# Optimization experiments

Measured on AMD Instinct MI355X. Metric: run time of the kernel, lower is better.

The kernel has to match this reference:

```python
import jax, jax.numpy as jnp
import numpy as np

B, D, E, K, NC, NH = 8192, 1280, 4, 2, 20, 4
CD = D // NC      # chunk_dim = 64
HD = CD // NH     # head_dim = 16
FF = CD * 4       # ffn hidden = 256
EPS = 1e-8


def setup_inputs() -> dict:
    key = jax.random.key(0)
    ks = jax.random.split(key, 12)
    f = lambda k, sh, s=0.02: jax.random.normal(k, sh, jnp.float32) * s
    return {
        "x": jax.random.normal(ks[0], (B, D), jnp.float32),
        "gate_w1": f(ks[1], (E * 4, D)), "gate_b1": jnp.zeros((E * 4,), jnp.float32),
        "gate_w2": f(ks[2], (E, E * 4)), "gate_b2": jnp.zeros((E,), jnp.float32),
        "pos_embed": f(ks[3], (E, NC, CD)),
        "norm1_g": jnp.ones((E, CD), jnp.float32),
        "in_proj_w": f(ks[4], (E, 3 * CD, CD)), "in_proj_b": jnp.zeros((E, 3 * CD), jnp.float32),
        "out_proj_w": f(ks[5], (E, CD, CD)), "out_proj_b": jnp.zeros((E, CD), jnp.float32),
        "ls1_g": jnp.full((E, CD), 1e-4, jnp.float32),
        "norm2_g": jnp.ones((E, CD), jnp.float32),
        "ffn_w1": f(ks[6], (E, FF, CD)), "ffn_b1": jnp.zeros((E, FF), jnp.float32),
        "ffn_w2": f(ks[7], (E, CD, FF)), "ffn_b2": jnp.zeros((E, CD), jnp.float32),
        "ls2_g": jnp.full((E, CD), 1e-4, jnp.float32),
        "proj_w": f(ks[8], (E, D, D)), "proj_b": jnp.zeros((E, D), jnp.float32),
    }


def _rms(v, g):
    # torch RMSNorm in source: x / (||x||_2 * dim^-0.5 + eps) * g
    n = jnp.linalg.norm(v, axis=-1, keepdims=True) * (CD ** -0.5)
    return v / (n + EPS) * g


def _expert(x, pos, n1g, ipw, ipb, opw, opb, l1, n2g, fw1, fb1, fw2, fb2, l2, pw, pb):
    b = x.shape[0]
    xs = x.reshape(b, NC, CD) + pos            # [b, NC, CD]
    xn = _rms(xs, n1g)
    qkv = xn @ ipw.T + ipb                      # [b, NC, 3*CD]
    q, k, v = jnp.split(qkv, 3, axis=-1)
    q = q.reshape(b, NC, NH, HD).transpose(0, 2, 1, 3)
    k = k.reshape(b, NC, NH, HD).transpose(0, 2, 1, 3)
    v = v.reshape(b, NC, NH, HD).transpose(0, 2, 1, 3)
    att = jax.nn.softmax(jnp.einsum('bhqd,bhkd->bhqk', q, k) * (HD ** -0.5), axis=-1)
    o = jnp.einsum('bhqk,bhkd->bhqd', att, v).transpose(0, 2, 1, 3).reshape(b, NC, CD)
    o = o @ opw.T + opb
    xs = xs + l1 * o                            # residual + LayerScale
    h = jax.nn.relu(_rms(xs, n2g) @ fw1.T + fb1) @ fw2.T + fb2
    xs = xs + l2 * h
    return xs.reshape(b, D) @ pw.T + pb         # final proj [b, D]


def reference(x, gate_w1, gate_b1, gate_w2, gate_b2, pos_embed, norm1_g,
              in_proj_w, in_proj_b, out_proj_w, out_proj_b, ls1_g, norm2_g,
              ffn_w1, ffn_b1, ffn_w2, ffn_b2, ls2_g, proj_w, proj_b):
    logits = jnp.tanh(x @ gate_w1.T + gate_b1) @ gate_w2.T + gate_b2   # [B, E]
    scores = jax.nn.softmax(logits, axis=-1)
    tk_s, tk_i = jax.lax.top_k(scores, K)
    tk_s = tk_s / (tk_s.sum(-1, keepdims=True) + 1e-6)
    onehot = jax.nn.one_hot(tk_i, E, dtype=x.dtype)                    # [B, K, E]
    w = (onehot * tk_s[..., None]).sum(1)                              # [B, E] combine weights
    eout = jax.vmap(_expert, in_axes=(None,) + (0,) * 15)(
        x, pos_embed, norm1_g, in_proj_w, in_proj_b, out_proj_w, out_proj_b,
        ls1_g, norm2_g, ffn_w1, ffn_b1, ffn_w2, ffn_b2, ls2_g, proj_w, proj_b)  # [E, B, D]
    output = jnp.einsum('ebd,be->bd', eout, w)
    aux_loss = jnp.float32(0.0)  # eval mode
    load = onehot.sum((0, 1))    # [E]
    return output, aux_loss, load
```

## Files before the change

### kernel.cpp

```cpp
#include <hip/hip_runtime.h>
#include <hip/hip_bf16.h>
#include <math.h>

#define B_SZ 8192
#define D_SZ 1280
#define NE   4
#define NC   20
#define CD   64
#define NH   4
#define HD   16
#define FF   256

typedef __attribute__((ext_vector_type(8))) short bf16x8;
typedef __attribute__((ext_vector_type(4))) float f32x4;

__device__ inline unsigned int pk2(float lo, float hi) {
    union { __hip_bfloat16 h; unsigned short s; } a, b;
    a.h = __float2bfloat16(lo); b.h = __float2bfloat16(hi);
    return (unsigned int)a.s | ((unsigned int)b.s << 16);
}
__device__ inline __hip_bfloat16 us2bf(unsigned short u) {
    union { unsigned short s; __hip_bfloat16 h; } c; c.s = u; return c.h;
}

#define WS_TOPI   256
#define WS_TOPW   (WS_TOPI + 2*B_SZ*4)
#define WS_IDX    (WS_TOPW + 2*B_SZ*4)
#define WS_WGT    (WS_IDX  + 2*B_SZ*4)
#define WS_ER0    (WS_WGT  + 2*B_SZ*4)
#define WS_ER1    (WS_ER0  + B_SZ*4)
#define WS_PRK    (WS_ER1  + B_SZ*4)
#define WS_BBE    (WS_PRK  + B_SZ*4)
#define WS_BBP    (WS_BBE  + 32*4*4)
#define WS_PRA    (WS_BBP  + 32*16*4)
#define WS_PRB    (WS_PRA  + (B_SZ+128)*4)
#define WS_PW1    (WS_PRB  + (B_SZ+128)*4)
#define WS_PW2    (WS_PW1  + (B_SZ+128)*4)
#define WS_PRW    (WS_PW2  + (B_SZ+128)*4)
#define WS_XSF    532480
#define XSF_ROWS  (2*B_SZ + 128)
#define WS_PWB    (WS_XSF + (size_t)XSF_ROWS * D_SZ * 2)
#define WS_IPWB   (WS_PWB  + (size_t)NE * D_SZ * D_SZ * 2)
#define WS_OPWB   (WS_IPWB + (size_t)NE * 192 * 64 * 2)
#define WS_FW1B   (WS_OPWB + (size_t)NE * 64 * 64 * 2)
#define WS_FW2B   (WS_FW1B + (size_t)NE * 256 * 64 * 2)

__global__ __launch_bounds__(256) void convert_pw(const float* __restrict__ pw,
                                                  __hip_bfloat16* __restrict__ pwb)
{
    size_t i = ((size_t)blockIdx.x * 256 + threadIdx.x) * 8;
    float4 a = *(const float4*)(pw + i);
    float4 b = *(const float4*)(pw + i + 4);
    __hip_bfloat16 h[8];
    h[0] = __float2bfloat16(a.x); h[1] = __float2bfloat16(a.y);
    h[2] = __float2bfloat16(a.z); h[3] = __float2bfloat16(a.w);
    h[4] = __float2bfloat16(b.x); h[5] = __float2bfloat16(b.y);
    h[6] = __float2bfloat16(b.z); h[7] = __float2bfloat16(b.w);
    *(uint4*)(pwb + i) = *(uint4*)h;
}

#define N_IPW (NE*192*64)
#define N_OPW (NE*64*64)
#define N_FW1 (NE*256*64)
#define N_FW2 (NE*64*256)
__global__ __launch_bounds__(256) void convert_small(
    const float* __restrict__ ipw, const float* __restrict__ opw,
    const float* __restrict__ fw1, const float* __restrict__ fw2,
    __hip_bfloat16* __restrict__ ipwb, __hip_bfloat16* __restrict__ opwb,
    __hip_bfloat16* __restrict__ fw1b, __hip_bfloat16* __restrict__ fw2b)
{
    size_t i = ((size_t)blockIdx.x * 256 + threadIdx.x) * 8;
    const float* src; __hip_bfloat16* dst; size_t off;
    if (i < N_IPW)                       { src = ipw; dst = ipwb; off = i; }
    else if (i < N_IPW + N_OPW)          { src = opw; dst = opwb; off = i - N_IPW; }
    else if (i < N_IPW + N_OPW + N_FW1)  { src = fw1; dst = fw1b; off = i - N_IPW - N_OPW; }
    else                                 { src = fw2; dst = fw2b; off = i - N_IPW - N_OPW - N_FW1; }
    float4 a = *(const float4*)(src + off);
    float4 b = *(const float4*)(src + off + 4);
    __hip_bfloat16 h[8];
    h[0] = __float2bfloat16(a.x); h[1] = __float2bfloat16(a.y);
    h[2] = __float2bfloat16(a.z); h[3] = __float2bfloat16(a.w);
    h[4] = __float2bfloat16(b.x); h[5] = __float2bfloat16(b.y);
    h[6] = __float2bfloat16(b.z); h[7] = __float2bfloat16(b.w);
    *(uint4*)(dst + off) = *(uint4*)h;
}

__global__ __launch_bounds__(64) void gate_kernel(
    const float* __restrict__ x, const float* __restrict__ gw1, const float* __restrict__ gb1,
    const float* __restrict__ gw2, const float* __restrict__ gb2,
    int* __restrict__ topi, float* __restrict__ topw)
{
    const int b = blockIdx.x;
    const int lane = threadIdx.x;
    float acc[16];
#pragma unroll
    for (int j = 0; j < 16; ++j) acc[j] = 0.f;
    const float* xr = x + (size_t)b * D_SZ;
    for (int t = 0; t < NC; ++t) {
        float xv = xr[t * 64 + lane];
#pragma unroll
        for (int j = 0; j < 16; ++j) acc[j] += xv * gw1[j * D_SZ + t * 64 + lane];
    }
#pragma unroll
    for (int j = 0; j < 16; ++j) {
        acc[j] += __shfl_xor(acc[j], 32, 64);
        acc[j] += __shfl_xor(acc[j], 16, 64);
        acc[j] += __shfl_xor(acc[j], 8, 64);
        acc[j] += __shfl_xor(acc[j], 4, 64);
        acc[j] += __shfl_xor(acc[j], 2, 64);
        acc[j] += __shfl_xor(acc[j], 1, 64);
    }
    if (lane == 0) {
        float h[16];
#pragma unroll
        for (int j = 0; j < 16; ++j) h[j] = tanhf(acc[j] + gb1[j]);
        float l[4];
#pragma unroll
        for (int e = 0; e < 4; ++e) {
            float sv = gb2[e];
#pragma unroll
            for (int j = 0; j < 16; ++j) sv += h[j] * gw2[e * 16 + j];
            l[e] = sv;
        }
        float m = fmaxf(fmaxf(l[0], l[1]), fmaxf(l[2], l[3]));
        float p[4];
        float sum = 0.f;
#pragma unroll
        for (int e = 0; e < 4; ++e) { p[e] = expf(l[e] - m); sum += p[e]; }
#pragma unroll
        for (int e = 0; e < 4; ++e) p[e] /= sum;
        int i1 = 0;
#pragma unroll
        for (int e = 1; e < 4; ++e) if (p[e] > p[i1]) i1 = e;
        int i2 = (i1 == 0) ? 1 : 0;
#pragma unroll
        for (int e = 0; e < 4; ++e) if (e != i1 && p[e] > p[i2]) i2 = e;
        float s1 = p[i1], s2 = p[i2];
        float denom = s1 + s2 + 1e-6f;
        topi[b * 2 + 0] = i1;
        topi[b * 2 + 1] = i2;
        topw[b * 2 + 0] = s1 / denom;
        topw[b * 2 + 1] = s2 / denom;
    }
}

__global__ __launch_bounds__(256) void count_kernel(
    const int* __restrict__ topi,
    int* __restrict__ cnt, int* __restrict__ pcnt,
    int* __restrict__ er0, int* __restrict__ er1, int* __restrict__ prk,
    int* __restrict__ bbe, int* __restrict__ bbp)
{
    __shared__ int he[4], hp[16];
    const int t = threadIdx.x;
    const int blk = blockIdx.x;
    const int b = blk * 256 + t;
    if (t < 4) he[t] = 0;
    if (t < 16) hp[t] = 0;
    __syncthreads();
    int e0 = topi[b * 2], e1 = topi[b * 2 + 1];
    er0[b] = atomicAdd(&he[e0], 1);
    er1[b] = atomicAdd(&he[e1], 1);
    prk[b] = atomicAdd(&hp[e0 * 4 + e1], 1);
    __syncthreads();
    if (t < 4)  bbe[blk * 4 + t]  = atomicAdd(&cnt[t], he[t]);
    if (t < 16) bbp[blk * 16 + t] = atomicAdd(&pcnt[t], hp[t]);
}

__global__ void offsets_kernel(const int* __restrict__ cnt, const int* __restrict__ pcnt,
                               int* __restrict__ offA, int* __restrict__ poff,
                               float* __restrict__ load_out)
{
    if (threadIdx.x == 0 && blockIdx.x == 0) {
        int a = 0;
#pragma unroll
        for (int e = 0; e < 4; ++e) { offA[e] = a; a += cnt[e]; }
        offA[4] = a;
        int q = 0;
#pragma unroll
        for (int p = 0; p < 16; ++p) { poff[p] = q; q += pcnt[p]; }
        poff[16] = q;
#pragma unroll
        for (int e = 0; e < 4; ++e) load_out[e] = (float)cnt[e];
    }
}

__global__ __launch_bounds__(256) void fill_kernel(
    const int* __restrict__ topi, const float* __restrict__ topw,
    const int* __restrict__ offA, const int* __restrict__ poff,
    const int* __restrict__ er0, const int* __restrict__ er1, const int* __restrict__ prk,
    const int* __restrict__ bbe, const int* __restrict__ bbp,
    int* __restrict__ idx_list, float* __restrict__ wgt_list,
    int* __restrict__ prA, int* __restrict__ prB,
    float* __restrict__ pw1, float* __restrict__ pw2, int* __restrict__ prow)
{
    const int b = blockIdx.x * 256 + threadIdx.x;
    const int blk = blockIdx.x;
    int e0 = topi[b * 2], e1 = topi[b * 2 + 1];
    float w0 = topw[b * 2], w1 = topw[b * 2 + 1];
    int slot0 = offA[e0] + bbe[blk * 4 + e0] + er0[b];
    int slot1 = offA[e1] + bbe[blk * 4 + e1] + er1[b];
    idx_list[slot0] = b; wgt_list[slot0] = w0;
    idx_list[slot1] = b; wgt_list[slot1] = w1;
    int p = e0 * 4 + e1;
    int pos = poff[p] + bbp[blk * 16 + p] + prk[b];
    prA[pos] = slot0; prB[pos] = slot1;
    pw1[pos] = w0; pw2[pos] = w1; prow[pos] = b;
}

__global__ __launch_bounds__(256, 5) void expert_inner(
    const float* __restrict__ x, const float* __restrict__ pos,
    const float* __restrict__ n1g,
    const __hip_bfloat16* __restrict__ ipwb, const float* __restrict__ ipb,
    const __hip_bfloat16* __restrict__ opwb, const float* __restrict__ opb,
    const float* __restrict__ ls1, const float* __restrict__ n2g,
    const __hip_bfloat16* __restrict__ fw1b, const float* __restrict__ fb1,
    const __hip_bfloat16* __restrict__ fw2b, const float* __restrict__ fb2,
    const float* __restrict__ ls2,
    const int* __restrict__ offA, const int* __restrict__ idx_list,
    const float* __restrict__ wgt_list,
    __hip_bfloat16* __restrict__ xsf)
{
    __shared__ __hip_bfloat16 s_big[4][32][72];

    const int t = threadIdx.x;
    const int w = t >> 6;
    const int lane = t & 63;
    const int l15 = lane & 15, lg = lane >> 4;
    const int s = blockIdx.x * 4 + w;
    const int e = (s >= offA[1]) + (s >= offA[2]) + (s >= offA[3]);
    const int b = idx_list[s];
    const float wgt = wgt_list[s];

    __hip_bfloat16 (* const big)[72] = s_big[w];

    const float* xg = x + (size_t)b * D_SZ;
    const float* pg = pos + (size_t)e * D_SZ;
    const __hip_bfloat16* ipw_e = ipwb + (size_t)e * 192 * 64;
    const float* ipb_e = ipb + e * 192;

    f32x4 xsr[2][4];

#pragma unroll
    for (int mt = 0; mt < 2; ++mt)
#pragma unroll
        for (int r = 0; r < 4; ++r) {
            const int row = mt * 16 + lg * 4 + r;
#pragma unroll
            for (int nt = 0; nt < 4; ++nt) {
                float v = 0.f;
                if (row < NC) v = xg[row * 64 + nt * 16 + l15] + pg[row * 64 + nt * 16 + l15];
                xsr[mt][nt][r] = v;
            }
        }
    {
        float g1[4];
#pragma unroll
        for (int nt = 0; nt < 4; ++nt) g1[nt] = n1g[e * CD + nt * 16 + l15];
#pragma unroll
        for (int mt = 0; mt < 2; ++mt)
#pragma unroll
            for (int r = 0; r < 4; ++r) {
                const int row = mt * 16 + lg * 4 + r;
                float ss = 0.f;
#pragma unroll
                for (int nt = 0; nt < 4; ++nt) ss += xsr[mt][nt][r] * xsr[mt][nt][r];
                ss += __shfl_xor(ss, 1); ss += __shfl_xor(ss, 2);
                ss += __shfl_xor(ss, 4); ss += __shfl_xor(ss, 8);
                float inv = __builtin_amdgcn_rcpf(sqrtf(ss) * 0.125f + 1e-8f);
#pragma unroll
                for (int nt = 0; nt < 4; ++nt)
                    big[row][nt * 16 + l15] = __float2bfloat16(xsr[mt][nt][r] * inv * g1[nt]);
            }
    }

    bf16x8 af[2][2];
#pragma unroll
    for (int mt = 0; mt < 2; ++mt)
#pragma unroll
        for (int ks = 0; ks < 2; ++ks)
            af[mt][ks] = *(const bf16x8*)&big[mt * 16 + l15][ks * 32 + lg * 8];

    unsigned int opk[NH][4];
#pragma unroll
    for (int h = 0; h < NH; ++h) {
        const int nq = h * 16 + l15;
        f32x4 qa[2], ka[2], va[2];
#pragma unroll
        for (int mt = 0; mt < 2; ++mt) { qa[mt] = (f32x4){0,0,0,0}; ka[mt] = (f32x4){0,0,0,0}; va[mt] = (f32x4){0,0,0,0}; }
#pragma unroll
        for (int ks = 0; ks < 2; ++ks) {
            bf16x8 wq = *(const bf16x8*)(ipw_e + (size_t)(nq) * 64 + ks * 32 + lg * 8);
            bf16x8 wk = *(const bf16x8*)(ipw_e + (size_t)(64 + nq) * 64 + ks * 32 + lg * 8);
            bf16x8 wv = *(const bf16x8*)(ipw_e + (size_t)(128 + nq) * 64 + ks * 32 + lg * 8);
#pragma unroll
            for (int mt = 0; mt < 2; ++mt) {
                qa[mt] = __builtin_amdgcn_mfma_f32_16x16x32_bf16(af[mt][ks], wq, qa[mt], 0, 0, 0);
                ka[mt] = __builtin_amdgcn_mfma_f32_16x16x32_bf16(af[mt][ks], wk, ka[mt], 0, 0, 0);
                va[mt] = __builtin_amdgcn_mfma_f32_16x16x32_bf16(af[mt][ks], wv, va[mt], 0, 0, 0);
            }
        }
        const float biq = ipb_e[nq], bik = ipb_e[64 + nq], biv = ipb_e[128 + nq];

        unsigned int vp0[2], vp1[2];
#pragma unroll
        for (int mt = 0; mt < 2; ++mt) {
            vp0[mt] = pk2(va[mt][0] + biv, va[mt][1] + biv);
            vp1[mt] = pk2(va[mt][2] + biv, va[mt][3] + biv);
        }
        const int aA = (((lg & 1) * 32) + l15) * 4;
        const int aB = aA + 64;
        int d0a = __builtin_amdgcn_ds_bpermute(aA, (int)vp0[0]);
        int d0b = __builtin_amdgcn_ds_bpermute(aA, (int)vp0[1]);
        int d1a = __builtin_amdgcn_ds_bpermute(aA, (int)vp1[0]);
        int d1b = __builtin_amdgcn_ds_bpermute(aA, (int)vp1[1]);
        int d2a = __builtin_amdgcn_ds_bpermute(aB, (int)vp0[0]);
        int d2b = __builtin_amdgcn_ds_bpermute(aB, (int)vp0[1]);
        int d3a = __builtin_amdgcn_ds_bpermute(aB, (int)vp1[0]);
        int d3b = __builtin_amdgcn_ds_bpermute(aB, (int)vp1[1]);
        const bool hi2 = (lg >= 2);
        union { int i[4]; bf16x8 v; } uv;
        uv.i[0] = hi2 ? d0b : d0a;
        uv.i[1] = hi2 ? d1b : d1a;
        uv.i[2] = hi2 ? d2b : d2a;
        uv.i[3] = hi2 ? d3b : d3a;
        const bf16x8 bv = uv.v;

#pragma unroll
        for (int mt = 0; mt < 2; ++mt)
#pragma unroll
            for (int r = 0; r < 4; ++r) {
                const int row = mt * 16 + lg * 4 + r;
                big[row][l15]      = __float2bfloat16(qa[mt][r] + biq);
                big[row][16 + l15] = __float2bfloat16(ka[mt][r] + bik);
            }

        bf16x8 aq[2], bk[2];
        const bf16x8 zf = {0,0,0,0,0,0,0,0};
#pragma unroll
        for (int mt = 0; mt < 2; ++mt) {
            aq[mt] = zf;
            if (lg < 2) aq[mt] = *(const bf16x8*)&big[mt * 16 + l15][lg * 8];
        }
#pragma unroll
        for (int nt = 0; nt < 2; ++nt) {
            bk[nt] = zf;
            if (lg < 2) bk[nt] = *(const bf16x8*)&big[nt * 16 + l15][16 + lg * 8];
        }

        f32x4 sc[2][2];
#pragma unroll
        for (int mt = 0; mt < 2; ++mt)
#pragma unroll
            for (int nt = 0; nt < 2; ++nt)
                sc[mt][nt] = __builtin_amdgcn_mfma_f32_16x16x32_bf16(aq[mt], bk[nt], (f32x4){0,0,0,0}, 0, 0, 0);

#pragma unroll
        for (int mt = 0; mt < 2; ++mt)
#pragma unroll
            for (int r = 0; r < 4; ++r) {
                float e0 = __expf(sc[mt][0][r] * 0.25f);
                float e1 = (l15 < 4) ? __expf(sc[mt][1][r] * 0.25f) : 0.f;
                float sm = e0 + e1;
                sm += __shfl_xor(sm, 1); sm += __shfl_xor(sm, 2);
                sm += __shfl_xor(sm, 4); sm += __shfl_xor(sm, 8);
                float is = __builtin_amdgcn_rcpf(sm);
                const int row = mt * 16 + lg * 4 + r;
                big[row][l15]      = __float2bfloat16(e0 * is);
                big[row][16 + l15] = __float2bfloat16((l15 < 4) ? e1 * is : 0.f);
            }

#pragma unroll
        for (int mt = 0; mt < 2; ++mt) {
            bf16x8 ap = *(const bf16x8*)&big[mt * 16 + l15][lg * 8];
            f32x4 o = __builtin_amdgcn_mfma_f32_16x16x32_bf16(ap, bv, (f32x4){0,0,0,0}, 0, 0, 0);
            opk[h][mt * 2 + 0] = pk2(o[0], o[1]);
            opk[h][mt * 2 + 1] = pk2(o[2], o[3]);
        }
    }

#pragma unroll
    for (int h = 0; h < NH; ++h)
#pragma unroll
        for (int mt = 0; mt < 2; ++mt) {
            const int row0 = mt * 16 + lg * 4;
            const int col = h * 16 + l15;
            big[row0 + 0][col] = us2bf((unsigned short)(opk[h][mt * 2 + 0] & 0xffff));
            big[row0 + 1][col] = us2bf((unsigned short)(opk[h][mt * 2 + 0] >> 16));
            big[row0 + 2][col] = us2bf((unsigned short)(opk[h][mt * 2 + 1] & 0xffff));
            big[row0 + 3][col] = us2bf((unsigned short)(opk[h][mt * 2 + 1] >> 16));
        }

    const __hip_bfloat16* opw_e = opwb + (size_t)e * 64 * 64;
    {
        bf16x8 aO[2][2];
#pragma unroll
        for (int mt = 0; mt < 2; ++mt)
#pragma unroll
            for (int ks = 0; ks < 2; ++ks)
                aO[mt][ks] = *(const bf16x8*)&big[mt * 16 + l15][ks * 32 + lg * 8];
#pragma unroll
        for (int nt = 0; nt < 4; ++nt) {
            const int n = nt * 16 + l15;
            f32x4 po[2] = {{0,0,0,0},{0,0,0,0}};
#pragma unroll
            for (int ks = 0; ks < 2; ++ks) {
                bf16x8 bw = *(const bf16x8*)(opw_e + (size_t)n * 64 + ks * 32 + lg * 8);
#pragma unroll
                for (int mt = 0; mt < 2; ++mt)
                    po[mt] = __builtin_amdgcn_mfma_f32_16x16x32_bf16(aO[mt][ks], bw, po[mt], 0, 0, 0);
            }
            const float lv = ls1[e * 64 + n], ob = opb[e * 64 + n];
#pragma unroll
            for (int mt = 0; mt < 2; ++mt)
#pragma unroll
                for (int r = 0; r < 4; ++r)
                    xsr[mt][nt][r] += lv * (po[mt][r] + ob);
        }
    }

    {
        float g2[4];
#pragma unroll
        for (int nt = 0; nt < 4; ++nt) g2[nt] = n2g[e * CD + nt * 16 + l15];
#pragma unroll
        for (int mt = 0; mt < 2; ++mt)
#pragma unroll
            for (int r = 0; r < 4; ++r) {
                const int row = mt * 16 + lg * 4 + r;
                float ss = 0.f;
#pragma unroll
                for (int nt = 0; nt < 4; ++nt) ss += xsr[mt][nt][r] * xsr[mt][nt][r];
                ss += __shfl_xor(ss, 1); ss += __shfl_xor(ss, 2);
                ss += __shfl_xor(ss, 4); ss += __shfl_xor(ss, 8);
                float inv = __builtin_amdgcn_rcpf(sqrtf(ss) * 0.125f + 1e-8f);
#pragma unroll
                for (int nt = 0; nt < 4; ++nt)
                    big[row][nt * 16 + l15] = __float2bfloat16(xsr[mt][nt][r] * inv * g2[nt]);
            }
    }

    {
        bf16x8 af2[2][2];
#pragma unroll
        for (int mt = 0; mt < 2; ++mt)
#pragma unroll
            for (int ks = 0; ks < 2; ++ks)
                af2[mt][ks] = *(const bf16x8*)&big[mt * 16 + l15][ks * 32 + lg * 8];

        f32x4 a2[2][4];
#pragma unroll
        for (int mt = 0; mt < 2; ++mt)
#pragma unroll
            for (int nt = 0; nt < 4; ++nt) a2[mt][nt] = (f32x4){0,0,0,0};

        const __hip_bfloat16* f1_e = fw1b + (size_t)e * 256 * 64;
        const float* fb1_e = fb1 + e * 256;
        const __hip_bfloat16* f2_e = fw2b + (size_t)e * 64 * 256;

#pragma unroll
        for (int c = 0; c < 8; ++c) {
            const int cb = (c & 1) * 32;
#pragma unroll
            for (int ntc = 0; ntc < 2; ++ntc) {
                const int n = c * 32 + ntc * 16 + l15;
                f32x4 hc[2] = {{0,0,0,0},{0,0,0,0}};
#pragma unroll
                for (int ks = 0; ks < 2; ++ks) {
                    bf16x8 bw = *(const bf16x8*)(f1_e + (size_t)n * 64 + ks * 32 + lg * 8);
#pragma unroll
                    for (int mt = 0; mt < 2; ++mt)
                        hc[mt] = __builtin_amdgcn_mfma_f32_16x16x32_bf16(af2[mt][ks], bw, hc[mt], 0, 0, 0);
                }
                const float b1 = fb1_e[n];
#pragma unroll
                for (int mt = 0; mt < 2; ++mt)
#pragma unroll
                    for (int r = 0; r < 4; ++r)
                        big[mt * 16 + lg * 4 + r][cb + ntc * 16 + l15] =
                            __float2bfloat16(fmaxf(hc[mt][r] + b1, 0.f));
            }
            bf16x8 ah[2];
#pragma unroll
            for (int mt = 0; mt < 2; ++mt)
                ah[mt] = *(const bf16x8*)&big[mt * 16 + l15][cb + lg * 8];
#pragma unroll
            for (int nt = 0; nt < 4; ++nt) {
                bf16x8 w2 = *(const bf16x8*)(f2_e + (size_t)(nt * 16 + l15) * 256 + c * 32 + lg * 8);
#pragma unroll
                for (int mt = 0; mt < 2; ++mt)
                    a2[mt][nt] = __builtin_amdgcn_mfma_f32_16x16x32_bf16(ah[mt], w2, a2[mt][nt], 0, 0, 0);
            }
        }

#pragma unroll
        for (int nt = 0; nt < 4; ++nt) {
            const int n = nt * 16 + l15;
            const float lv = ls2[e * 64 + n], b2 = fb2[e * 64 + n];
#pragma unroll
            for (int mt = 0; mt < 2; ++mt)
#pragma unroll
                for (int r = 0; r < 4; ++r)
                    xsr[mt][nt][r] += lv * (a2[mt][nt][r] + b2);
        }
    }

#pragma unroll
    for (int mt = 0; mt < 2; ++mt)
#pragma unroll
        for (int r = 0; r < 4; ++r) {
            const int row = mt * 16 + lg * 4 + r;
            if (row < NC) {
#pragma unroll
                for (int nt = 0; nt < 4; ++nt)
                    big[row][nt * 16 + l15] = __float2bfloat16(wgt * xsr[mt][nt][r]);
            }
        }
    __hip_bfloat16* xo = xsf + (size_t)s * D_SZ;
#pragma unroll
    for (int it = 0; it < 3; ++it) {
        const int c2 = lane + it * 64;
        if (c2 < 160) {
            const int row = c2 >> 3, off = (c2 & 7) * 8;
            bf16x8 v = *(const bf16x8*)&big[row][off];
            *(bf16x8*)(xo + row * 64 + off) = v;
        }
    }
}

#define PROWP 130

__global__ __launch_bounds__(256) void proj_pair(
    const __hip_bfloat16* __restrict__ xsf, const __hip_bfloat16* __restrict__ pwb,
    const float* __restrict__ pb, const int* __restrict__ poff,
    const int* __restrict__ prA, const int* __restrict__ prB,
    const float* __restrict__ pw1, const float* __restrict__ pw2,
    const int* __restrict__ prow, float* __restrict__ out)
{
    __shared__ short As[8][PROWP][8];
    __shared__ short Bs[8][PROWP][8];
    __shared__ int   sSlot[2][128];
    __shared__ float sW[2][128];
    __shared__ int   sRow[128];

    int mblk = blockIdx.x;
    int p = 0, base = 0, M = 0;
#pragma unroll
    for (int pp = 0; pp < 16; ++pp) {
        int b0 = poff[pp], b1 = poff[pp + 1];
        int nb = (b1 - b0 + 127) >> 7;
        if (p == pp && mblk >= nb) { mblk -= nb; p = pp + 1; }
        else if (p == pp) { base = b0; M = b1 - b0; }
    }
    if (p >= 16) return;
    const int ea = p >> 2, eb = p & 3;

    const int m0 = mblk * 128;
    const int n0 = blockIdx.y * 128;
    const int t = threadIdx.x;
    const int w = t >> 6, lane = t & 63;
    const int wm = (w & 1) * 64, wn = (w >> 1) * 64;
    const int l15 = lane & 15, lg = lane >> 4;

    if (t < 128) {
        int posn = base + m0 + t;
        int sa = prA[posn], sb = prB[posn];
        sSlot[0][t] = min(max(sa, 0), 2 * B_SZ);
        sSlot[1][t] = min(max(sb, 0), 2 * B_SZ);
        sW[0][t] = pw1[posn]; sW[1][t] = pw2[posn];
        sRow[t] = prow[posn];
    }
    __syncthreads();

    f32x4 acc[4][4];
#pragma unroll
    for (int i = 0; i < 4; ++i)
#pragma unroll
        for (int j = 0; j < 4; ++j) acc[i][j] = (f32x4){0.f, 0.f, 0.f, 0.f};

    const int arow0 = t >> 3;
    const int akb = t & 7;

#pragma unroll
    for (int ph = 0; ph < 2; ++ph) {
        const __hip_bfloat16* Bg = pwb + (size_t)(ph ? eb : ea) * D_SZ * D_SZ + (size_t)n0 * D_SZ;
        int aslot[4];
#pragma unroll
        for (int i = 0; i < 4; ++i) aslot[i] = sSlot[ph][arow0 + 32 * i];

        for (int kt = 0; kt < D_SZ; kt += 64) {
            __syncthreads();
#pragma unroll
            for (int i = 0; i < 4; ++i) {
                int row = arow0 + 32 * i;
                *(uint4*)&As[akb][row][0] =
                    *(const uint4*)(xsf + (size_t)aslot[i] * D_SZ + kt + akb * 8);
                *(uint4*)&Bs[akb][row][0] =
                    *(const uint4*)(Bg + (size_t)row * D_SZ + kt + akb * 8);
            }
            __syncthreads();
#pragma unroll
            for (int ks = 0; ks < 2; ++ks) {
                int kb = ks * 4 + lg;
                bf16x8 af[4], bfr[4];
#pragma unroll
                for (int ti = 0; ti < 4; ++ti) af[ti]  = *(const bf16x8*)&As[kb][wm + ti * 16 + l15][0];
#pragma unroll
                for (int tj = 0; tj < 4; ++tj) bfr[tj] = *(const bf16x8*)&Bs[kb][wn + tj * 16 + l15][0];
#pragma unroll
                for (int ti = 0; ti < 4; ++ti)
#pragma unroll
                    for (int tj = 0; tj < 4; ++tj)
                        acc[ti][tj] = __builtin_amdgcn_mfma_f32_16x16x32_bf16(
                            af[ti], bfr[tj], acc[ti][tj], 0, 0, 0);
            }
        }
    }

    float pbva[4], pbvb[4];
#pragma unroll
    for (int tj = 0; tj < 4; ++tj) {
        int nc = n0 + wn + tj * 16 + l15;
        pbva[tj] = pb[(size_t)ea * D_SZ + nc];
        pbvb[tj] = pb[(size_t)eb * D_SZ + nc];
    }

#pragma unroll
    for (int ti = 0; ti < 4; ++ti) {
#pragma unroll
        for (int r = 0; r < 4; ++r) {
            int m = wm + ti * 16 + lg * 4 + r;
            if (m0 + m < M) {
                float w1 = sW[0][m], w2 = sW[1][m];
                float* orow = out + (size_t)sRow[m] * D_SZ + n0 + wn + l15;
#pragma unroll
                for (int tj = 0; tj < 4; ++tj)
                    orow[tj * 16] = acc[ti][tj][r] + w1 * pbva[tj] + w2 * pbvb[tj];
            }
        }
    }
}

extern "C" void kernel_launch(void* const* d_in, const int* in_sizes, int n_in,
                              void* d_out, int out_size, void* d_ws, size_t ws_size,
                              hipStream_t stream)
{
    const float* x   = (const float*)d_in[0];
    const float* gw1 = (const float*)d_in[1];
    const float* gb1 = (const float*)d_in[2];
    const float* gw2 = (const float*)d_in[3];
    const float* gb2 = (const float*)d_in[4];
    const float* pos = (const float*)d_in[5];
    const float* n1g = (const float*)d_in[6];
    const float* ipw = (const float*)d_in[7];
    const float* ipb = (const float*)d_in[8];
    const float* opw = (const float*)d_in[9];
    const float* opb = (const float*)d_in[10];
    const float* ls1 = (const float*)d_in[11];
    const float* n2g = (const float*)d_in[12];
    const float* fw1 = (const float*)d_in[13];
    const float* fb1 = (const float*)d_in[14];
    const float* fw2 = (const float*)d_in[15];
    const float* fb2 = (const float*)d_in[16];
    const float* ls2 = (const float*)d_in[17];
    const float* pw  = (const float*)d_in[18];
    const float* pb  = (const float*)d_in[19];

    float* out = (float*)d_out;

    char* ws = (char*)d_ws;
    int*   cnt      = (int*)(ws + 0);
    int*   pcnt     = (int*)(ws + 16);
    int*   offA     = (int*)(ws + 80);
    int*   poff     = (int*)(ws + 112);
    int*   topi     = (int*)(ws + WS_TOPI);
    float* topw     = (float*)(ws + WS_TOPW);
    int*   idx_list = (int*)(ws + WS_IDX);
    float* wgt_list = (float*)(ws + WS_WGT);
    int*   er0      = (int*)(ws + WS_ER0);
    int*   er1      = (int*)(ws + WS_ER1);
    int*   prk      = (int*)(ws + WS_PRK);
    int*   bbe      = (int*)(ws + WS_BBE);
    int*   bbp      = (int*)(ws + WS_BBP);
    int*   prA      = (int*)(ws + WS_PRA);
    int*   prB      = (int*)(ws + WS_PRB);
    float* pw1      = (float*)(ws + WS_PW1);
    float* pw2      = (float*)(ws + WS_PW2);
    int*   prow     = (int*)(ws + WS_PRW);
    __hip_bfloat16* xsf  = (__hip_bfloat16*)(ws + WS_XSF);
    __hip_bfloat16* pwb  = (__hip_bfloat16*)(ws + WS_PWB);
    __hip_bfloat16* ipwb = (__hip_bfloat16*)(ws + WS_IPWB);
    __hip_bfloat16* opwb = (__hip_bfloat16*)(ws + WS_OPWB);
    __hip_bfloat16* fw1b = (__hip_bfloat16*)(ws + WS_FW1B);
    __hip_bfloat16* fw2b = (__hip_bfloat16*)(ws + WS_FW2B);

    hipMemsetAsync(d_ws, 0, 256, stream);
    hipMemsetAsync(out + (size_t)B_SZ * D_SZ, 0, 5 * sizeof(float), stream);

    float* load_out = out + (size_t)B_SZ * D_SZ + 1;

    convert_pw<<<NE * D_SZ * D_SZ / (256 * 8), 256, 0, stream>>>(pw, pwb);
    convert_small<<<(N_IPW + N_OPW + N_FW1 + N_FW2) / (256 * 8), 256, 0, stream>>>(
        ipw, opw, fw1, fw2, ipwb, opwb, fw1b, fw2b);
    gate_kernel<<<B_SZ, 64, 0, stream>>>(x, gw1, gb1, gw2, gb2, topi, topw);
    count_kernel<<<B_SZ / 256, 256, 0, stream>>>(topi, cnt, pcnt, er0, er1, prk, bbe, bbp);
    offsets_kernel<<<1, 64, 0, stream>>>(cnt, pcnt, offA, poff, load_out);
    fill_kernel<<<B_SZ / 256, 256, 0, stream>>>(topi, topw, offA, poff, er0, er1, prk,
                                                bbe, bbp, idx_list, wgt_list,
                                                prA, prB, pw1, pw2, prow);
    expert_inner<<<(2 * B_SZ) / 4, 256, 0, stream>>>(x, pos, n1g, ipwb, ipb, opwb, opb, ls1,
                                                     n2g, fw1b, fb1, fw2b, fb2, ls2,
                                                     offA, idx_list, wgt_list, xsf);
    proj_pair<<<dim3(96, D_SZ / 128), 256, 0, stream>>>(
        xsf, pwb, pb, poff, prA, prB, pw1, pw2, prow, out);
}
```

Baseline: 569.7 us.

## Fold LayerScale into out/FFN2 weights and accumulate projections into residual

Pre-scales the out_proj and ffn_w2 rows by the LayerScale gammas during bf16 conversion, so the MFMA outputs can accumulate straight into the residual registers instead of separate accumulators followed by a scale-and-add. The out-projection is now done per head inside the attention loop, using the head's output staged in shared memory, which removes the opk packing buffer. Q/K staging is moved ahead of the V projection to shorten live ranges, and the launch-bounds occupancy hint drops from 5 to 4 blocks. Per-head out-proj MFMAs use only half-filled K (zeros in lg>=2 lanes), so MFMA work on that stage doubles. Folding a small gamma (1e-4) into bf16 weights may shift rounding.

```diff
diff --git a/kernel.cpp b/kernel.cpp
--- a/kernel.cpp
+++ b/kernel.cpp
@@ -18,9 +18,6 @@
     union { __hip_bfloat16 h; unsigned short s; } a, b;
     a.h = __float2bfloat16(lo); b.h = __float2bfloat16(hi);
     return (unsigned int)a.s | ((unsigned int)b.s << 16);
-}
-__device__ inline __hip_bfloat16 us2bf(unsigned short u) {
-    union { unsigned short s; __hip_bfloat16 h; } c; c.s = u; return c.h;
 }
 
 #define WS_TOPI   256
@@ -66,22 +63,32 @@
 __global__ __launch_bounds__(256) void convert_small(
     const float* __restrict__ ipw, const float* __restrict__ opw,
     const float* __restrict__ fw1, const float* __restrict__ fw2,
+    const float* __restrict__ ls1, const float* __restrict__ ls2,
     __hip_bfloat16* __restrict__ ipwb, __hip_bfloat16* __restrict__ opwb,
     __hip_bfloat16* __restrict__ fw1b, __hip_bfloat16* __restrict__ fw2b)
 {
     size_t i = ((size_t)blockIdx.x * 256 + threadIdx.x) * 8;
     const float* src; __hip_bfloat16* dst; size_t off;
+    float scale = 1.f;
     if (i < N_IPW)                       { src = ipw; dst = ipwb; off = i; }
-    else if (i < N_IPW + N_OPW)          { src = opw; dst = opwb; off = i - N_IPW; }
+    else if (i < N_IPW + N_OPW)          {
+        off = i - N_IPW; src = opw; dst = opwb;
+        int e = (int)(off >> 12); int n = (int)((off >> 6) & 63);
+        scale = ls1[e * 64 + n];
+    }
     else if (i < N_IPW + N_OPW + N_FW1)  { src = fw1; dst = fw1b; off = i - N_IPW - N_OPW; }
-    else                                 { src = fw2; dst = fw2b; off = i - N_IPW - N_OPW - N_FW1; }
+    else {
+        off = i - N_IPW - N_OPW - N_FW1; src = fw2; dst = fw2b;
+        int e = (int)(off >> 14); int n = (int)((off >> 8) & 63);
+        scale = ls2[e * 64 + n];
+    }
     float4 a = *(const float4*)(src + off);
     float4 b = *(const float4*)(src + off + 4);
     __hip_bfloat16 h[8];
-    h[0] = __float2bfloat16(a.x); h[1] = __float2bfloat16(a.y);
-    h[2] = __float2bfloat16(a.z); h[3] = __float2bfloat16(a.w);
-    h[4] = __float2bfloat16(b.x); h[5] = __float2bfloat16(b.y);
-    h[6] = __float2bfloat16(b.z); h[7] = __float2bfloat16(b.w);
+    h[0] = __float2bfloat16(a.x * scale); h[1] = __float2bfloat16(a.y * scale);
+    h[2] = __float2bfloat16(a.z * scale); h[3] = __float2bfloat16(a.w * scale);
+    h[4] = __float2bfloat16(b.x * scale); h[5] = __float2bfloat16(b.y * scale);
+    h[6] = __float2bfloat16(b.z * scale); h[7] = __float2bfloat16(b.w * scale);
     *(uint4*)(dst + off) = *(uint4*)h;
 }
 
@@ -207,7 +214,7 @@
     pw1[pos] = w0; pw2[pos] = w1; prow[pos] = b;
 }
 
-__global__ __launch_bounds__(256, 5) void expert_inner(
+__global__ __launch_bounds__(256, 4) void expert_inner(
     const float* __restrict__ x, const float* __restrict__ pos,
     const float* __restrict__ n1g,
     const __hip_bfloat16* __restrict__ ipwb, const float* __restrict__ ipb,
@@ -280,26 +287,44 @@
         for (int ks = 0; ks < 2; ++ks)
             af[mt][ks] = *(const bf16x8*)&big[mt * 16 + l15][ks * 32 + lg * 8];
 
-    unsigned int opk[NH][4];
+    const __hip_bfloat16* opw_e = opwb + (size_t)e * 64 * 64;
+    const bf16x8 zf = {0,0,0,0,0,0,0,0};
+
 #pragma unroll
     for (int h = 0; h < NH; ++h) {
         const int nq = h * 16 + l15;
-        f32x4 qa[2], ka[2], va[2];
-#pragma unroll
-        for (int mt = 0; mt < 2; ++mt) { qa[mt] = (f32x4){0,0,0,0}; ka[mt] = (f32x4){0,0,0,0}; va[mt] = (f32x4){0,0,0,0}; }
+
+        f32x4 qa[2] = {{0,0,0,0},{0,0,0,0}};
+        f32x4 ka[2] = {{0,0,0,0},{0,0,0,0}};
 #pragma unroll
         for (int ks = 0; ks < 2; ++ks) {
             bf16x8 wq = *(const bf16x8*)(ipw_e + (size_t)(nq) * 64 + ks * 32 + lg * 8);
             bf16x8 wk = *(const bf16x8*)(ipw_e + (size_t)(64 + nq) * 64 + ks * 32 + lg * 8);
-            bf16x8 wv = *(const bf16x8*)(ipw_e + (size_t)(128 + nq) * 64 + ks * 32 + lg * 8);
 #pragma unroll
             for (int mt = 0; mt < 2; ++mt) {
                 qa[mt] = __builtin_amdgcn_mfma_f32_16x16x32_bf16(af[mt][ks], wq, qa[mt], 0, 0, 0);
                 ka[mt] = __builtin_amdgcn_mfma_f32_16x16x32_bf16(af[mt][ks], wk, ka[mt], 0, 0, 0);
+            }
+        }
+        const float biq = ipb_e[nq], bik = ipb_e[64 + nq];
+#pragma unroll
+        for (int mt = 0; mt < 2; ++mt)
+#pragma unroll
+            for (int r = 0; r < 4; ++r) {
+                const int row = mt * 16 + lg * 4 + r;
+                big[row][l15]      = __float2bfloat16(qa[mt][r] + biq);
+                big[row][16 + l15] = __float2bfloat16(ka[mt][r] + bik);
+            }
+
+        f32x4 va[2] = {{0,0,0,0},{0,0,0,0}};
+#pragma unroll
+        for (int ks = 0; ks < 2; ++ks) {
+            bf16x8 wv = *(const bf16x8*)(ipw_e + (size_t)(128 + nq) * 64 + ks * 32 + lg * 8);
+#pragma unroll
+            for (int mt = 0; mt < 2; ++mt)
                 va[mt] = __builtin_amdgcn_mfma_f32_16x16x32_bf16(af[mt][ks], wv, va[mt], 0, 0, 0);
-            }
-        }
-        const float biq = ipb_e[nq], bik = ipb_e[64 + nq], biv = ipb_e[128 + nq];
+        }
+        const float biv = ipb_e[128 + nq];
 
         unsigned int vp0[2], vp1[2];
 #pragma unroll
@@ -325,17 +350,7 @@
         uv.i[3] = hi2 ? d3b : d3a;
         const bf16x8 bv = uv.v;
 
-#pragma unroll
-        for (int mt = 0; mt < 2; ++mt)
-#pragma unroll
-            for (int r = 0; r < 4; ++r) {
-                const int row = mt * 16 + lg * 4 + r;
-                big[row][l15]      = __float2bfloat16(qa[mt][r] + biq);
-                big[row][16 + l15] = __float2bfloat16(ka[mt][r] + bik);
-            }
-
         bf16x8 aq[2], bk[2];
-        const bf16x8 zf = {0,0,0,0,0,0,0,0};
 #pragma unroll
         for (int mt = 0; mt < 2; ++mt) {
             aq[mt] = zf;
@@ -346,7 +361,6 @@
             bk[nt] = zf;
             if (lg < 2) bk[nt] = *(const bf16x8*)&big[nt * 16 + l15][16 + lg * 8];
         }
-
         f32x4 sc[2][2];
 #pragma unroll
         for (int mt = 0; mt < 2; ++mt)
@@ -373,55 +387,39 @@
         for (int mt = 0; mt < 2; ++mt) {
             bf16x8 ap = *(const bf16x8*)&big[mt * 16 + l15][lg * 8];
             f32x4 o = __builtin_amdgcn_mfma_f32_16x16x32_bf16(ap, bv, (f32x4){0,0,0,0}, 0, 0, 0);
-            opk[h][mt * 2 + 0] = pk2(o[0], o[1]);
-            opk[h][mt * 2 + 1] = pk2(o[2], o[3]);
-        }
-    }
-
-#pragma unroll
-    for (int h = 0; h < NH; ++h)
+#pragma unroll
+            for (int r = 0; r < 4; ++r)
+                big[mt * 16 + lg * 4 + r][32 + l15] = __float2bfloat16(o[r]);
+        }
+
+        bf16x8 aOh[2];
 #pragma unroll
         for (int mt = 0; mt < 2; ++mt) {
-            const int row0 = mt * 16 + lg * 4;
-            const int col = h * 16 + l15;
-            big[row0 + 0][col] = us2bf((unsigned short)(opk[h][mt * 2 + 0] & 0xffff));
-            big[row0 + 1][col] = us2bf((unsigned short)(opk[h][mt * 2 + 0] >> 16));
-            big[row0 + 2][col] = us2bf((unsigned short)(opk[h][mt * 2 + 1] & 0xffff));
-            big[row0 + 3][col] = us2bf((unsigned short)(opk[h][mt * 2 + 1] >> 16));
-        }
-
-    const __hip_bfloat16* opw_e = opwb + (size_t)e * 64 * 64;
+            aOh[mt] = zf;
+            if (lg < 2) aOh[mt] = *(const bf16x8*)&big[mt * 16 + l15][32 + lg * 8];
+        }
+#pragma unroll
+        for (int nt = 0; nt < 4; ++nt) {
+            bf16x8 bw = zf;
+            if (lg < 2) bw = *(const bf16x8*)(opw_e + (size_t)(nt * 16 + l15) * 64 + h * 16 + lg * 8);
+#pragma unroll
+            for (int mt = 0; mt < 2; ++mt)
+                xsr[mt][nt] = __builtin_amdgcn_mfma_f32_16x16x32_bf16(aOh[mt], bw, xsr[mt][nt], 0, 0, 0);
+        }
+    }
+
     {
-        bf16x8 aO[2][2];
-#pragma unroll
-        for (int mt = 0; mt < 2; ++mt)
-#pragma unroll
-            for (int ks = 0; ks < 2; ++ks)
-                aO[mt][ks] = *(const bf16x8*)&big[mt * 16 + l15][ks * 32 + lg * 8];
+        float g2[4];
 #pragma unroll
         for (int nt = 0; nt < 4; ++nt) {
             const int n = nt * 16 + l15;
-            f32x4 po[2] = {{0,0,0,0},{0,0,0,0}};
-#pragma unroll
-            for (int ks = 0; ks < 2; ++ks) {
-                bf16x8 bw = *(const bf16x8*)(opw_e + (size_t)n * 64 + ks * 32 + lg * 8);
-#pragma unroll
-                for (int mt = 0; mt < 2; ++mt)
-                    po[mt] = __builtin_amdgcn_mfma_f32_16x16x32_bf16(aO[mt][ks], bw, po[mt], 0, 0, 0);
-            }
-            const float lv = ls1[e * 64 + n], ob = opb[e * 64 + n];
+            const float ob1 = ls1[e * 64 + n] * opb[e * 64 + n];
+            g2[nt] = n2g[e * CD + n];
 #pragma unroll
             for (int mt = 0; mt < 2; ++mt)
 #pragma unroll
-                for (int r = 0; r < 4; ++r)
-                    xsr[mt][nt][r] += lv * (po[mt][r] + ob);
-        }
-    }
-
-    {
-        float g2[4];
-#pragma unroll
-        for (int nt = 0; nt < 4; ++nt) g2[nt] = n2g[e * CD + nt * 16 + l15];
+                for (int r = 0; r < 4; ++r) xsr[mt][nt][r] += ob1;
+        }
 #pragma unroll
         for (int mt = 0; mt < 2; ++mt)
 #pragma unroll
@@ -447,12 +445,6 @@
             for (int ks = 0; ks < 2; ++ks)
                 af2[mt][ks] = *(const bf16x8*)&big[mt * 16 + l15][ks * 32 + lg * 8];
 
-        f32x4 a2[2][4];
-#pragma unroll
-        for (int mt = 0; mt < 2; ++mt)
-#pragma unroll
-            for (int nt = 0; nt < 4; ++nt) a2[mt][nt] = (f32x4){0,0,0,0};
-
         const __hip_bfloat16* f1_e = fw1b + (size_t)e * 256 * 64;
         const float* fb1_e = fb1 + e * 256;
         const __hip_bfloat16* f2_e = fw2b + (size_t)e * 64 * 256;
@@ -488,19 +480,18 @@
                 bf16x8 w2 = *(const bf16x8*)(f2_e + (size_t)(nt * 16 + l15) * 256 + c * 32 + lg * 8);
 #pragma unroll
                 for (int mt = 0; mt < 2; ++mt)
-                    a2[mt][nt] = __builtin_amdgcn_mfma_f32_16x16x32_bf16(ah[mt], w2, a2[mt][nt], 0, 0, 0);
+                    xsr[mt][nt] = __builtin_amdgcn_mfma_f32_16x16x32_bf16(ah[mt], w2, xsr[mt][nt], 0, 0, 0);
             }
         }
 
 #pragma unroll
         for (int nt = 0; nt < 4; ++nt) {
             const int n = nt * 16 + l15;
-            const float lv = ls2[e * 64 + n], b2 = fb2[e * 64 + n];
+            const float b2s = ls2[e * 64 + n] * fb2[e * 64 + n];
 #pragma unroll
             for (int mt = 0; mt < 2; ++mt)
 #pragma unroll
-                for (int r = 0; r < 4; ++r)
-                    xsr[mt][nt][r] += lv * (a2[mt][nt][r] + b2);
+                for (int r = 0; r < 4; ++r) xsr[mt][nt][r] += b2s;
         }
     }
 
@@ -700,7 +691,7 @@
 
     convert_pw<<<NE * D_SZ * D_SZ / (256 * 8), 256, 0, stream>>>(pw, pwb);
     convert_small<<<(N_IPW + N_OPW + N_FW1 + N_FW2) / (256 * 8), 256, 0, stream>>>(
-        ipw, opw, fw1, fw2, ipwb, opwb, fw1b, fw2b);
+        ipw, opw, fw1, fw2, ls1, ls2, ipwb, opwb, fw1b, fw2b);
     gate_kernel<<<B_SZ, 64, 0, stream>>>(x, gw1, gb1, gw2, gb2, topi, topw);
     count_kernel<<<B_SZ / 256, 256, 0, stream>>>(topi, cnt, pcnt, er0, er1, prk, bbe, bbp);
     offsets_kernel<<<1, 64, 0, stream>>>(cnt, pcnt, offA, poff, load_out);
```

Result: faster. 508.4 us (-10.8%).
